# Optimization experiments

Hardware: AMD Instinct MI355X
Metric: run time of the kernel (lower is better)

## Reference

```python
import jax, jax.numpy as jnp
import numpy as np

EPS = 1e-5

def _conv1x1_bn(x, W, b, g, beta):
    # 1x1 conv == channel matmul; BN in training mode uses batch stats over (N,H,W)
    y = jnp.einsum('bchw,oc->bohw', x, W) + b[None, :, None, None]
    mu = jnp.mean(y, axis=(0, 2, 3))
    var = jnp.var(y, axis=(0, 2, 3))
    y = (y - mu[None, :, None, None]) * jax.lax.rsqrt(var + EPS)[None, :, None, None]
    return y * g[None, :, None, None] + beta[None, :, None, None]


def setup_inputs() -> dict:
    key = jax.random.key(0)
    ks = jax.random.split(key, 7)
    b, c, h, w = 8, 256, 64, 64
    sc = 1.0 / np.sqrt(c)
    inp = {
        'x': jax.random.normal(ks[0], (b, c, h, w), jnp.float32),
        'Wq': jax.random.normal(ks[1], (c, c), jnp.float32) * sc,
        'bq': jax.random.normal(ks[2], (c,), jnp.float32) * 0.02,
        'gq': jnp.ones((c,), jnp.float32),
        'betaq': jnp.zeros((c,), jnp.float32),
        'Wk': jax.random.normal(ks[3], (c, c), jnp.float32) * sc,
        'bk': jax.random.normal(ks[4], (c,), jnp.float32) * 0.02,
        'gk': jnp.ones((c,), jnp.float32),
        'betak': jnp.zeros((c,), jnp.float32),
        'Wv': jax.random.normal(ks[5], (c, c), jnp.float32) * sc,
        'bv': jax.random.normal(ks[6], (c,), jnp.float32) * 0.02,
        'gv': jnp.ones((c,), jnp.float32),
        'betav': jnp.zeros((c,), jnp.float32),
    }
    return inp


def reference(x, Wq, bq, gq, betaq, Wk, bk, gk, betak, Wv, bv, gv, betav):
    b, c, h, w = x.shape
    scale = float(h) ** (-0.5)
    Q = _conv1x1_bn(x, Wq, bq, gq, betaq).reshape(b, c, h * w)
    K = _conv1x1_bn(x, Wk, bk, gk, betak).reshape(b, c, h * w)
    V = _conv1x1_bn(x, Wv, bv, gv, betav).reshape(b, c, h * w)
    # un-normalized attention (no softmax)
    pixelMap = jnp.einsum('bcq,bck->bqk', Q, K) * scale  # [b, N, N]
    out = jnp.einsum('bqk,bck->bcq', pixelMap, V)        # [b, c, N]
    return out.reshape(b, c, h, w)
```

## Files before the change

### kernel.cpp

```cpp
#include <hip/hip_runtime.h>
#include <hip/hip_bf16.h>


#define BB 8
#define CC 256
#define NPIX 4096
#define PTOT 32768
#define EPSV 1e-5f
#define SCALEV 0.125f

#define OFF_PG    0L
#define OFF_SP    6291456L
#define OFF_S     6324224L
#define OFF_GHAT  6326272L
#define OFF_XBAR  6391808L
#define OFF_WP    6392064L
#define OFF_WKTF  6588672L
#define OFF_WVTF  6654208L
#define OFF_CVEC  6719744L
#define OFF_ACC   6720512L
#define OFF_GBF   6732800L
#define OFF_WQT   6994944L
#define OFF_WKT   7027712L
#define OFF_WVB   7060480L
#define OFF_ZT    7093248L
#define OFF_FT    7126016L
#define OFF_TBF   7388160L

#define ACC_U    0
#define ACC_W    2048
#define ACC_Y    4096
#define ACC_R    4352
#define ACC_H    4608
#define ACC_G    6656
#define ACC_VG   8704
#define ACC_SCAL 10752
#define ACC_TOT  12288

typedef __attribute__((ext_vector_type(8))) short short8;
typedef __attribute__((ext_vector_type(4))) float f32x4;

#define MFMA16(a, b, c) __builtin_amdgcn_mfma_f32_16x16x32_bf16((a), (b), (c), 0, 0, 0)

__device__ __forceinline__ ushort f2bf(float f) {
    union { float f; unsigned u; } v; v.f = f;
    const unsigned r = (v.u + 0x7FFFu + ((v.u >> 16) & 1u)) >> 16;
    return (ushort)r;
}

__device__ __forceinline__ float bf2f(ushort u) {
    union { unsigned u; float f; } v; v.u = ((unsigned)u) << 16;
    return v.f;
}

__device__ __forceinline__ ushort2 f2bf2(float a, float b) {
    __hip_bfloat162 h = __float22bfloat162_rn(float2{a, b});
    union { __hip_bfloat162 h; ushort2 u; } v; v.h = h;
    return v.u;
}

__device__ __forceinline__ float block_reduce(float v, float* red, int tid) {
    red[tid] = v; __syncthreads();
    for (int st = 128; st > 0; st >>= 1) {
        if (tid < st) red[tid] += red[tid + st];
        __syncthreads();
    }
    float r = red[0]; __syncthreads();
    return r;
}

__device__ __forceinline__ float2 wred2(float a, float b, float* red8, int tid) {
    #pragma unroll
    for (int s = 32; s > 0; s >>= 1) {
        a += __shfl_xor(a, s);
        b += __shfl_xor(b, s);
    }
    if ((tid & 63) == 0) { red8[(tid >> 6) * 2] = a; red8[(tid >> 6) * 2 + 1] = b; }
    __syncthreads();
    const float ra = red8[0] + red8[2] + red8[4] + red8[6];
    const float rb = red8[1] + red8[3] + red8[5] + red8[7];
    __syncthreads();
    return float2{ra, rb};
}

__global__ __launch_bounds__(256, 2) void gram_mfma(const float* __restrict__ x,
                                                    float* __restrict__ Pg,
                                                    float* __restrict__ Sp,
                                                    float* __restrict__ Ghat,
                                                    float* __restrict__ Acc) {
    __shared__ __align__(16) ushort Ab[128 * 72];
    __shared__ __align__(16) ushort Bb[128 * 72];
    __shared__ float rs[128];
    const int tid = threadIdx.x;
    const int ks = blockIdx.x, b = blockIdx.y, tt = blockIdx.z;
    const int lb = (tt * 8 + b) * 16 + ks;
    if (lb < 64) {
        #pragma unroll
        for (int i = 0; i < 4; ++i) Ghat[lb * 1024 + i * 256 + tid] = 0.f;
    } else if (lb < 76) {
        const int base = (lb - 64) * 1024;
        #pragma unroll
        for (int i = 0; i < 4; ++i) Acc[base + i * 256 + tid] = 0.f;
    }
    const int it = (tt == 1) ? 1 : 0;
    const int jt = (tt == 0) ? 0 : 1;
    const bool diag = (tt < 2);
    const int i0 = it * 128, j0 = jt * 128, k0 = ks * 256;
    const float* xb = x + (long)b * CC * NPIX;
    const int c = tid & 15, rp = tid >> 4;
    const int wave = tid >> 6, lane = tid & 63;
    const int wr = (wave >> 1) * 64, wc = (wave & 1) * 64;
    const int m = lane & 15, q8 = (lane >> 4) * 8;

    if (tid < 128) rs[tid] = 0.f;
    float rloc[8] = {};
    f32x4 acc[4][4];
    #pragma unroll
    for (int a = 0; a < 4; ++a)
        #pragma unroll
        for (int q = 0; q < 4; ++q) acc[a][q] = (f32x4){0.f, 0.f, 0.f, 0.f};

    const float* Abase = xb + (long)i0 * NPIX + k0 + c * 4;
    const float* Bbase = xb + (long)j0 * NPIX + k0 + c * 4;

    float4 va[8], vb[8];
    #pragma unroll
    for (int pp = 0; pp < 8; ++pp)
        va[pp] = *(const float4*)&Abase[(long)(pp * 16 + rp) * NPIX];
    if (!diag) {
        #pragma unroll
        for (int pp = 0; pp < 8; ++pp)
            vb[pp] = *(const float4*)&Bbase[(long)(pp * 16 + rp) * NPIX];
    }

    for (int kc = 0; kc < 256; kc += 64) {
        __syncthreads();
        #pragma unroll
        for (int pp = 0; pp < 8; ++pp) {
            const int row = pp * 16 + rp;
            const float4 v = va[pp];
            rloc[pp] += v.x + v.y + v.z + v.w;
            const ushort2 w01 = f2bf2(v.x, v.y);
            const ushort2 w23 = f2bf2(v.z, v.w);
            ushort4 w; w.x = w01.x; w.y = w01.y; w.z = w23.x; w.w = w23.y;
            *(ushort4*)&Ab[row * 72 + c * 4] = w;
        }
        if (!diag) {
            #pragma unroll
            for (int pp = 0; pp < 8; ++pp) {
                const int row = pp * 16 + rp;
                const float4 v = vb[pp];
                const ushort2 w01 = f2bf2(v.x, v.y);
                const ushort2 w23 = f2bf2(v.z, v.w);
                ushort4 w; w.x = w01.x; w.y = w01.y; w.z = w23.x; w.w = w23.y;
                *(ushort4*)&Bb[row * 72 + c * 4] = w;
            }
        }
        const int kn = kc + 64;
        if (kn < 256) {
            #pragma unroll
            for (int pp = 0; pp < 8; ++pp)
                va[pp] = *(const float4*)&Abase[(long)(pp * 16 + rp) * NPIX + kn];
            if (!diag) {
                #pragma unroll
                for (int pp = 0; pp < 8; ++pp)
                    vb[pp] = *(const float4*)&Bbase[(long)(pp * 16 + rp) * NPIX + kn];
            }
        }
        __syncthreads();
        const ushort* Bsrc = diag ? Ab : Bb;
        #pragma unroll
        for (int kk = 0; kk < 2; ++kk) {
            short8 af[4], bfv[4];
            #pragma unroll
            for (int a = 0; a < 4; ++a)
                af[a] = *(const short8*)&Ab[(wr + a * 16 + m) * 72 + kk * 32 + q8];
            #pragma unroll
            for (int q = 0; q < 4; ++q)
                bfv[q] = *(const short8*)&Bsrc[(wc + q * 16 + m) * 72 + kk * 32 + q8];
            #pragma unroll
            for (int a = 0; a < 4; ++a)
                #pragma unroll
                for (int q = 0; q < 4; ++q)
                    acc[a][q] = MFMA16(af[a], bfv[q], acc[a][q]);
        }
    }
    if (diag) {
        #pragma unroll
        for (int pp = 0; pp < 8; ++pp) atomicAdd(&rs[pp * 16 + rp], rloc[pp]);
        __syncthreads();
        if (tid < 128) Sp[(((long)ks * 8 + b) * 2 + it) * 128 + tid] = rs[tid];
    }
    float* Pt = Pg + (((long)ks * 8 + b) * 3 + tt) * 16384;
    const int rq = (lane >> 4) * 4;
    #pragma unroll
    for (int a = 0; a < 4; ++a) {
        #pragma unroll
        for (int q = 0; q < 4; ++q) {
            const int col = wc + q * 16 + m;
            #pragma unroll
            for (int reg = 0; reg < 4; ++reg)
                Pt[(long)(wr + a * 16 + rq + reg) * 128 + col] = acc[a][q][reg];
        }
    }
}

__global__ __launch_bounds__(256) void reduce_mirror(const float* __restrict__ Pg,
                                                     const float* __restrict__ Sp,
                                                     ushort* __restrict__ Gbf,
                                                     float* __restrict__ Ghat,
                                                     float* __restrict__ S,
                                                     float* __restrict__ xbar) {
    const int blk = blockIdx.x, tid = threadIdx.x;
    if (blk == 384) {
        const int it2 = tid >> 7, rr = tid & 127;
        float xacc = 0.f;
        for (int b = 0; b < BB; ++b) {
            float acc = 0.f;
            #pragma unroll
            for (int ks = 0; ks < 16; ++ks)
                acc += Sp[(((long)ks * 8 + b) * 2 + it2) * 128 + rr];
            S[b * 256 + tid] = acc;
            xacc += acc;
        }
        xbar[tid] = xacc * (1.0f / PTOT);
        return;
    }
    __shared__ float tile[32][33];
    const int tt = blk >> 7;
    const int sub = (blk >> 3) & 15;
    const int b = blk & 7;
    const int sr = (sub >> 2) * 32, sc = (sub & 3) * 32;
    const int it = (tt == 1) ? 1 : 0;
    const int jt = (tt == 0) ? 0 : 1;
    const bool offd = (tt == 2);
    const int gi0 = it * 128 + sr, gj0 = jt * 128 + sc;
    const int r = tid >> 3, c4 = (tid & 7) * 4;
    const float inv = 1.0f / PTOT;

    float s0 = 0.f, s1 = 0.f, s2 = 0.f, s3 = 0.f;
    #pragma unroll
    for (int ks = 0; ks < 16; ++ks) {
        const float4 v = *(const float4*)&Pg[(((long)ks * 8 + b) * 3 + tt) * 16384
                                             + (long)(sr + r) * 128 + sc + c4];
        s0 += v.x; s1 += v.y; s2 += v.z; s3 += v.w;
    }
    ushort4 w;
    w.x = f2bf(s0); w.y = f2bf(s1); w.z = f2bf(s2); w.w = f2bf(s3);
    *(ushort4*)&Gbf[(long)b * 65536 + (long)(gi0 + r) * 256 + gj0 + c4] = w;
    float* gd = &Ghat[(long)(gi0 + r) * 256 + gj0 + c4];
    atomicAdd(gd + 0, s0 * inv);
    atomicAdd(gd + 1, s1 * inv);
    atomicAdd(gd + 2, s2 * inv);
    atomicAdd(gd + 3, s3 * inv);
    if (offd) {
        tile[r][c4 + 0] = s0; tile[r][c4 + 1] = s1;
        tile[r][c4 + 2] = s2; tile[r][c4 + 3] = s3;
        __syncthreads();
        const float t0 = tile[c4 + 0][r], t1 = tile[c4 + 1][r];
        const float t2 = tile[c4 + 2][r], t3 = tile[c4 + 3][r];
        ushort4 tw;
        tw.x = f2bf(t0); tw.y = f2bf(t1); tw.z = f2bf(t2); tw.w = f2bf(t3);
        *(ushort4*)&Gbf[(long)b * 65536 + (long)(gj0 + r) * 256 + gi0 + c4] = tw;
        float* gm = &Ghat[(long)(gj0 + r) * 256 + gi0 + c4];
        atomicAdd(gm + 0, t0 * inv);
        atomicAdd(gm + 1, t1 * inv);
        atomicAdd(gm + 2, t2 * inv);
        atomicAdd(gm + 3, t3 * inv);
    }
}

__global__ __launch_bounds__(256) void stats_quad(const float* __restrict__ Wq, const float* __restrict__ Wk,
                           const float* __restrict__ Wv, const float* __restrict__ Ghat,
                           const float* __restrict__ xbar,
                           const float* bq, const float* gq, const float* betaq,
                           const float* bk, const float* gk, const float* betak,
                           const float* bv, const float* gv, const float* betav,
                           float* __restrict__ Wp, float* __restrict__ cvec,
                           ushort* __restrict__ WqT, ushort* __restrict__ WkT,
                           ushort* __restrict__ Wvb, float* __restrict__ WkTf,
                           float* __restrict__ WvTf) {
    const int og = blockIdx.x, t = blockIdx.y, tid = threadIdx.x;
    const int o0 = og * 4;
    const float* Wt  = t == 0 ? Wq : (t == 1 ? Wk : Wv);
    const float* bt  = t == 0 ? bq : (t == 1 ? bk : bv);
    const float* gt  = t == 0 ? gq : (t == 1 ? gk : gv);
    const float* bet = t == 0 ? betaq : (t == 1 ? betak : betav);
    __shared__ float wrows[4][256];
    __shared__ float red8[8];
    #pragma unroll
    for (int i = 0; i < 4; ++i) wrows[i][tid] = Wt[(o0 + i) * 256 + tid];
    const float xb = xbar[tid];
    __syncthreads();
    const float* grow = Ghat + (long)tid * 256;
    float tj[4] = {0.f, 0.f, 0.f, 0.f};
    #pragma unroll 8
    for (int k = 0; k < 256; k += 4) {
        const float4 g = *(const float4*)&grow[k];
        #pragma unroll
        for (int i = 0; i < 4; ++i)
            tj[i] += g.x * wrows[i][k]     + g.y * wrows[i][k + 1]
                   + g.z * wrows[i][k + 2] + g.w * wrows[i][k + 3];
    }
    #pragma unroll
    for (int i = 0; i < 4; ++i) {
        const int o = o0 + i;
        const float wv = wrows[i][tid];
        const float2 qw = wred2(wv * tj[i], wv * xb, red8, tid);
        const float bo = bt[o];
        const float mu = qw.y + bo;
        const float var = qw.x + 2.f * bo * mu - bo * bo - mu * mu;
        const float a = gt[o] * rsqrtf(var + EPSV);
        const float wpv = a * wv;
        Wp[(long)t * 65536 + o * 256 + tid] = wpv;
        const ushort wb = f2bf(wpv);
        if (t == 0) {
            WqT[(long)tid * 256 + o] = wb;
        } else if (t == 1) {
            WkT[(long)tid * 256 + o] = wb;
            WkTf[(long)tid * 256 + o] = wpv;
        } else {
            Wvb[(long)o * 256 + tid] = wb;
            WvTf[(long)tid * 256 + o] = wpv;
        }
        if (tid == 0) cvec[t * 256 + o] = a * (bo - mu) + bet[o];
    }
}

__device__ __forceinline__ void gemm_tile0(const ushort* __restrict__ Ab,
                                           const ushort* __restrict__ Bb,
                                           ushort* __restrict__ Db,
                                           int m0, int n0, int tid) {
    const int wave = tid >> 6, lane = tid & 63;
    const int wr = (wave >> 1) * 64, wc = (wave & 1) * 64;
    const int m = lane & 15, q8 = (lane >> 4) * 8;
    f32x4 acc[4][4];
    #pragma unroll
    for (int a = 0; a < 4; ++a)
        #pragma unroll
        for (int q = 0; q < 4; ++q) acc[a][q] = (f32x4){0.f, 0.f, 0.f, 0.f};
    #pragma unroll
    for (int kk = 0; kk < 8; ++kk) {
        short8 af[4], bfv[4];
        #pragma unroll
        for (int a = 0; a < 4; ++a)
            af[a] = *(const short8*)&Ab[(long)(m0 + wr + a * 16 + m) * 256 + kk * 32 + q8];
        #pragma unroll
        for (int q = 0; q < 4; ++q)
            bfv[q] = *(const short8*)&Bb[(long)(n0 + wc + q * 16 + m) * 256 + kk * 32 + q8];
        #pragma unroll
        for (int a = 0; a < 4; ++a)
            #pragma unroll
            for (int q = 0; q < 4; ++q)
                acc[a][q] = MFMA16(af[a], bfv[q], acc[a][q]);
    }
    const int rq = (lane >> 4) * 4;
    #pragma unroll
    for (int a = 0; a < 4; ++a) {
        #pragma unroll
        for (int q = 0; q < 4; ++q) {
            const int col = n0 + wc + q * 16 + m;
            #pragma unroll
            for (int reg = 0; reg < 4; ++reg)
                Db[(long)col * 256 + (m0 + wr + a * 16 + rq + reg)] = f2bf(acc[a][q][reg]);
        }
    }
}

__global__ __launch_bounds__(256) void zmida(const ushort* __restrict__ WkT,
                                             const ushort* __restrict__ WqT,
                                             ushort* __restrict__ ZT,
                                             const float* __restrict__ Wp,
                                             const float* __restrict__ WkTf,
                                             const float* __restrict__ WvTf,
                                             const float* __restrict__ S,
                                             const float* __restrict__ cvec,
                                             float* __restrict__ Acc) {
    const int blk = blockIdx.x, tid = threadIdx.x;
    __shared__ float sa[64], sb[64];
    if (blk < 4) {
        gemm_tile0(WkT, WqT, ZT, (blk >> 1) * 128, (blk & 1) * 128, tid);
        return;
    }
    if (blk < 36) {
        const int b = (blk - 4) >> 2, j0 = ((blk - 4) & 3) * 64;
        if (tid < 64) sa[tid] = S[b * 256 + j0 + tid];
        __syncthreads();
        float uu = 0.f, ww = 0.f;
        #pragma unroll 8
        for (int i = 0; i < 64; ++i) {
            const float sv = sa[i];
            uu += WvTf[(long)(j0 + i) * 256 + tid] * sv;
            ww += WkTf[(long)(j0 + i) * 256 + tid] * sv;
        }
        atomicAdd(&Acc[ACC_U + b * 256 + tid], uu);
        atomicAdd(&Acc[ACC_W + b * 256 + tid], ww);
    } else {
        const int o0 = (blk - 36) * 64;
        if (tid < 64) { sa[tid] = cvec[o0 + tid]; sb[tid] = cvec[256 + o0 + tid]; }
        __syncthreads();
        float yy = 0.f, rr = 0.f;
        #pragma unroll 8
        for (int i = 0; i < 64; ++i) {
            yy += Wp[65536L + (long)(o0 + i) * 256 + tid] * sa[i];
            rr += Wp[(long)(o0 + i) * 256 + tid] * sb[i];
        }
        atomicAdd(&Acc[ACC_Y + tid], yy);
        atomicAdd(&Acc[ACC_R + tid], rr);
    }
}

__global__ __launch_bounds__(256) void bcF2(const ushort* __restrict__ Gbf,
                                            const ushort* __restrict__ ZT,
                                            ushort* __restrict__ FT,
                                            const float* __restrict__ Wp,
                                            const float* __restrict__ cvec,
                                            float* __restrict__ Acc) {
    const int blk = blockIdx.x, tid = threadIdx.x;
    __shared__ float sa[64];
    __shared__ float red[256];
    if (blk < 32) {
        const int bz = blk >> 2, t = blk & 3;
        gemm_tile0(Gbf + (long)bz * 65536, ZT, FT + (long)bz * 65536,
                   (t >> 1) * 128, (t & 1) * 128, tid);
        return;
    }
    if (blk < 64) {
        const int b = (blk - 32) >> 2, o0 = ((blk - 32) & 3) * 64;
        if (tid < 64) sa[tid] = Acc[ACC_W + b * 256 + o0 + tid];
        __syncthreads();
        float hh = 0.f;
        #pragma unroll 8
        for (int i = 0; i < 64; ++i)
            hh += Wp[(long)(o0 + i) * 256 + tid] * sa[i];
        atomicAdd(&Acc[ACC_H + b * 256 + tid], hh);
    } else if (blk < 96) {
        const int b = (blk - 64) >> 2, o0 = ((blk - 64) & 3) * 64;
        if (tid < 64) sa[tid] = Acc[ACC_Y + o0 + tid];
        __syncthreads();
        float gg = 0.f;
        #pragma unroll 8
        for (int i = 0; i < 64; ++i)
            gg += bf2f(Gbf[(long)b * 65536 + (long)(o0 + i) * 256 + tid]) * sa[i];
        atomicAdd(&Acc[ACC_G + b * 256 + tid], gg);
    } else {
        const float cq = cvec[tid], ck = cvec[256 + tid];
        const float dkq = block_reduce(cq * ck, red, tid);
        if (tid == 0) Acc[ACC_SCAL] = dkq;
        for (int b = 0; b < BB; ++b) {
            const float dwq = block_reduce(Acc[ACC_W + b * 256 + tid] * cq, red, tid);
            if (tid == 0) Acc[ACC_SCAL + 1 + b] = dwq;
        }
    }
}

__global__ __launch_bounds__(256) void tvg(const ushort* __restrict__ Wvb,
                                           const ushort* __restrict__ FT,
                                           ushort* __restrict__ Tbf,
                                           const float* __restrict__ WvTf,
                                           const float* __restrict__ cvec,
                                           float* __restrict__ Acc) {
    const int blk = blockIdx.x, tid = threadIdx.x;
    __shared__ float sa[64];
    if (blk < 32) {
        const int bz = blk >> 2, t = blk & 3;
        const int m0 = (t >> 1) * 128, n0 = (t & 1) * 128;
        const ushort* Fb = FT + (long)bz * 65536;
        const int wave = tid >> 6, lane = tid & 63;
        const int wr = (wave >> 1) * 64, wc = (wave & 1) * 64;
        const int m = lane & 15, q8 = (lane >> 4) * 8;
        f32x4 acc[4][4];
        #pragma unroll
        for (int a = 0; a < 4; ++a)
            #pragma unroll
            for (int q = 0; q < 4; ++q) acc[a][q] = (f32x4){0.f, 0.f, 0.f, 0.f};
        #pragma unroll
        for (int kk = 0; kk < 8; ++kk) {
            short8 af[4], bfv[4];
            #pragma unroll
            for (int a = 0; a < 4; ++a)
                af[a] = *(const short8*)&Wvb[(long)(m0 + wr + a * 16 + m) * 256 + kk * 32 + q8];
            #pragma unroll
            for (int q = 0; q < 4; ++q)
                bfv[q] = *(const short8*)&Fb[(long)(n0 + wc + q * 16 + m) * 256 + kk * 32 + q8];
            #pragma unroll
            for (int a = 0; a < 4; ++a)
                #pragma unroll
                for (int q = 0; q < 4; ++q)
                    acc[a][q] = MFMA16(af[a], bfv[q], acc[a][q]);
        }
        const int rq = (lane >> 4) * 4;
        #pragma unroll
        for (int a = 0; a < 4; ++a) {
            #pragma unroll
            for (int q = 0; q < 4; ++q) {
                const int col = n0 + wc + q * 16 + m;
                const float rv = Acc[ACC_R + col];
                const float t2 = Acc[ACC_H + bz * 256 + col] + 4096.0f * rv;
                #pragma unroll
                for (int reg = 0; reg < 4; ++reg) {
                    const int row = m0 + wr + a * 16 + rq + reg;
                    const float val = SCALEV * (acc[a][q][reg]
                                                + Acc[ACC_U + bz * 256 + row] * rv
                                                + cvec[512 + row] * t2);
                    Tbf[(long)bz * 65536 + (long)row * 256 + col] = f2bf(val);
                }
            }
        }
    } else {
        const int b = (blk - 32) >> 2, j0 = ((blk - 32) & 3) * 64;
        if (tid < 64) sa[tid] = Acc[ACC_G + b * 256 + j0 + tid];
        __syncthreads();
        float vg = 0.f;
        #pragma unroll 8
        for (int i = 0; i < 64; ++i)
            vg += WvTf[(long)(j0 + i) * 256 + tid] * sa[i];
        atomicAdd(&Acc[ACC_VG + b * 256 + tid], vg);
    }
}

__global__ __launch_bounds__(256) void out_mfma(const ushort* __restrict__ Tbf,
                                                const float* __restrict__ x,
                                                const float* __restrict__ Acc,
                                                const float* __restrict__ cvec,
                                                float* __restrict__ out) {
    __shared__ __align__(16) ushort Bs[64 * 264];
    const int tid = threadIdx.x;
    const int p0 = blockIdx.x * 64;
    const int b = blockIdx.y;
    const float* xb = x + (long)b * CC * NPIX;
    const ushort* Tb = Tbf + (long)b * 65536;
    const float dkq = Acc[ACC_SCAL];
    const float dwqb = Acc[ACC_SCAL + 1 + b];

    const int c = tid & 15, kq = tid >> 4;
    #pragma unroll
    for (int kt = 0; kt < 4; ++kt) {
        const int k4 = kt * 64 + kq * 4;
        const int p = c * 4;
        const float4 v0 = *(const float4*)&xb[(long)(k4 + 0) * NPIX + p0 + p];
        const float4 v1 = *(const float4*)&xb[(long)(k4 + 1) * NPIX + p0 + p];
        const float4 v2 = *(const float4*)&xb[(long)(k4 + 2) * NPIX + p0 + p];
        const float4 v3 = *(const float4*)&xb[(long)(k4 + 3) * NPIX + p0 + p];
        ushort2 a01, a23;
        ushort4 w;
        a01 = f2bf2(v0.x, v1.x); a23 = f2bf2(v2.x, v3.x);
        w.x = a01.x; w.y = a01.y; w.z = a23.x; w.w = a23.y;
        *(ushort4*)&Bs[(p + 0) * 264 + k4] = w;
        a01 = f2bf2(v0.y, v1.y); a23 = f2bf2(v2.y, v3.y);
        w.x = a01.x; w.y = a01.y; w.z = a23.x; w.w = a23.y;
        *(ushort4*)&Bs[(p + 1) * 264 + k4] = w;
        a01 = f2bf2(v0.z, v1.z); a23 = f2bf2(v2.z, v3.z);
        w.x = a01.x; w.y = a01.y; w.z = a23.x; w.w = a23.y;
        *(ushort4*)&Bs[(p + 2) * 264 + k4] = w;
        a01 = f2bf2(v0.w, v1.w); a23 = f2bf2(v2.w, v3.w);
        w.x = a01.x; w.y = a01.y; w.z = a23.x; w.w = a23.y;
        *(ushort4*)&Bs[(p + 3) * 264 + k4] = w;
    }
    __syncthreads();

    const int wave = tid >> 6, lane = tid & 63;
    const int wr = wave * 64;
    const int m = lane & 15, q8 = (lane >> 4) * 8;
    f32x4 acc[4][4];
    #pragma unroll
    for (int a = 0; a < 4; ++a)
        #pragma unroll
        for (int q = 0; q < 4; ++q) acc[a][q] = (f32x4){0.f, 0.f, 0.f, 0.f};

    #pragma unroll
    for (int kk = 0; kk < 8; ++kk) {
        short8 af[4], bfv[4];
        #pragma unroll
        for (int a = 0; a < 4; ++a)
            af[a] = *(const short8*)&Tb[(long)(wr + a * 16 + m) * 256 + kk * 32 + q8];
        #pragma unroll
        for (int q = 0; q < 4; ++q)
            bfv[q] = *(const short8*)&Bs[(q * 16 + m) * 264 + kk * 32 + q8];
        #pragma unroll
        for (int a = 0; a < 4; ++a)
            #pragma unroll
            for (int q = 0; q < 4; ++q)
                acc[a][q] = MFMA16(af[a], bfv[q], acc[a][q]);
    }

    const int rq = (lane >> 4) * 4;
    #pragma unroll
    for (int a = 0; a < 4; ++a) {
        #pragma unroll
        for (int reg = 0; reg < 4; ++reg) {
            const int row = wr + a * 16 + rq + reg;
            const float off_ = SCALEV * (Acc[ACC_VG + b * 256 + row]
                                         + Acc[ACC_U + b * 256 + row] * dkq
                                         + cvec[512 + row] * (dwqb + 4096.0f * dkq));
            float* orow = &out[((long)b * CC + row) * NPIX + p0];
            #pragma unroll
            for (int q = 0; q < 4; ++q)
                orow[q * 16 + m] = acc[a][q][reg] + off_;
        }
    }
}

extern "C" void kernel_launch(void* const* d_in, const int* in_sizes, int n_in,
                              void* d_out, int out_size, void* d_ws, size_t ws_size,
                              hipStream_t stream) {
    const float* x     = (const float*)d_in[0];
    const float* Wq    = (const float*)d_in[1];
    const float* bq    = (const float*)d_in[2];
    const float* gq    = (const float*)d_in[3];
    const float* betaq = (const float*)d_in[4];
    const float* Wk    = (const float*)d_in[5];
    const float* bk    = (const float*)d_in[6];
    const float* gk    = (const float*)d_in[7];
    const float* betak = (const float*)d_in[8];
    const float* Wv    = (const float*)d_in[9];
    const float* bv    = (const float*)d_in[10];
    const float* gv    = (const float*)d_in[11];
    const float* betav = (const float*)d_in[12];
    float* ws = (float*)d_ws;

    float*  Pg   = ws + OFF_PG;
    float*  Sp   = ws + OFF_SP;
    float*  S    = ws + OFF_S;
    float*  Ghat = ws + OFF_GHAT;
    float*  Xbar = ws + OFF_XBAR;
    float*  Wp   = ws + OFF_WP;
    float*  WkTf = ws + OFF_WKTF;
    float*  WvTf = ws + OFF_WVTF;
    float*  cvec = ws + OFF_CVEC;
    float*  Acc  = ws + OFF_ACC;
    ushort* Gbf  = (ushort*)(ws + OFF_GBF);
    ushort* WqT  = (ushort*)(ws + OFF_WQT);
    ushort* WkT  = (ushort*)(ws + OFF_WKT);
    ushort* Wvb  = (ushort*)(ws + OFF_WVB);
    ushort* ZT   = (ushort*)(ws + OFF_ZT);
    ushort* FT   = (ushort*)(ws + OFF_FT);
    ushort* Tbf  = (ushort*)(ws + OFF_TBF);

    gram_mfma<<<dim3(16, 8, 3), 256, 0, stream>>>(x, Pg, Sp, Ghat, Acc);
    reduce_mirror<<<385, 256, 0, stream>>>(Pg, Sp, Gbf, Ghat, S, Xbar);
    stats_quad<<<dim3(64, 3), 256, 0, stream>>>(Wq, Wk, Wv, Ghat, Xbar,
                                                bq, gq, betaq, bk, gk, betak,
                                                bv, gv, betav, Wp, cvec,
                                                WqT, WkT, Wvb, WkTf, WvTf);
    zmida<<<40, 256, 0, stream>>>(WkT, WqT, ZT, Wp, WkTf, WvTf, S, cvec, Acc);
    bcF2<<<97, 256, 0, stream>>>(Gbf, ZT, FT, Wp, cvec, Acc);
    tvg<<<64, 256, 0, stream>>>(Wvb, FT, Tbf, WvTf, cvec, Acc);
    out_mfma<<<dim3(64, 8), 256, 0, stream>>>(Tbf, x, Acc, cvec, (float*)d_out);
}
```

Baseline: 190.1 us.

## Load Gram MFMA fragments directly from global memory, bypassing LDS staging

The Gram kernel no longer stages x tiles through shared memory. Each lane loads its MFMA fragment rows straight from global memory as float4 pairs, packs them to bf16 in registers, and reduces row sums with wave shuffles. Partial Gram tiles are now stored transposed as vector f32x4 writes, and the reduce kernel reads and transposes them to match. This removes LDS traffic and barriers, but each wave re-reads overlapping rows from global or L2 and loses the explicit register prefetch pipeline.

```diff
diff --git a/kernel.cpp b/kernel.cpp
--- a/kernel.cpp
+++ b/kernel.cpp
@@ -59,6 +59,15 @@
     return v.u;
 }
 
+__device__ __forceinline__ short8 pack8(const float4 u0, const float4 u1) {
+    union { short8 s; ushort2 u2[4]; } t;
+    t.u2[0] = f2bf2(u0.x, u0.y);
+    t.u2[1] = f2bf2(u0.z, u0.w);
+    t.u2[2] = f2bf2(u1.x, u1.y);
+    t.u2[3] = f2bf2(u1.z, u1.w);
+    return t.s;
+}
+
 __device__ __forceinline__ float block_reduce(float v, float* red, int tid) {
     red[tid] = v; __syncthreads();
     for (int st = 128; st > 0; st >>= 1) {
@@ -88,8 +97,6 @@
                                                     float* __restrict__ Sp,
                                                     float* __restrict__ Ghat,
                                                     float* __restrict__ Acc) {
-    __shared__ __align__(16) ushort Ab[128 * 72];
-    __shared__ __align__(16) ushort Bb[128 * 72];
     __shared__ float rs[128];
     const int tid = threadIdx.x;
     const int ks = blockIdx.x, b = blockIdx.y, tt = blockIdx.z;
@@ -107,90 +114,60 @@
     const bool diag = (tt < 2);
     const int i0 = it * 128, j0 = jt * 128, k0 = ks * 256;
     const float* xb = x + (long)b * CC * NPIX;
-    const int c = tid & 15, rp = tid >> 4;
     const int wave = tid >> 6, lane = tid & 63;
     const int wr = (wave >> 1) * 64, wc = (wave & 1) * 64;
     const int m = lane & 15, q8 = (lane >> 4) * 8;
 
-    if (tid < 128) rs[tid] = 0.f;
-    float rloc[8] = {};
+    const float* Arow = xb + (long)i0 * NPIX + k0;
+    const float* Brow = xb + (long)(diag ? i0 : j0) * NPIX + k0;
+
     f32x4 acc[4][4];
     #pragma unroll
     for (int a = 0; a < 4; ++a)
         #pragma unroll
         for (int q = 0; q < 4; ++q) acc[a][q] = (f32x4){0.f, 0.f, 0.f, 0.f};
-
-    const float* Abase = xb + (long)i0 * NPIX + k0 + c * 4;
-    const float* Bbase = xb + (long)j0 * NPIX + k0 + c * 4;
-
-    float4 va[8], vb[8];
-    #pragma unroll
-    for (int pp = 0; pp < 8; ++pp)
-        va[pp] = *(const float4*)&Abase[(long)(pp * 16 + rp) * NPIX];
-    if (!diag) {
-        #pragma unroll
-        for (int pp = 0; pp < 8; ++pp)
-            vb[pp] = *(const float4*)&Bbase[(long)(pp * 16 + rp) * NPIX];
-    }
-
-    for (int kc = 0; kc < 256; kc += 64) {
-        __syncthreads();
-        #pragma unroll
-        for (int pp = 0; pp < 8; ++pp) {
-            const int row = pp * 16 + rp;
-            const float4 v = va[pp];
-            rloc[pp] += v.x + v.y + v.z + v.w;
-            const ushort2 w01 = f2bf2(v.x, v.y);
-            const ushort2 w23 = f2bf2(v.z, v.w);
-            ushort4 w; w.x = w01.x; w.y = w01.y; w.z = w23.x; w.w = w23.y;
-            *(ushort4*)&Ab[row * 72 + c * 4] = w;
-        }
-        if (!diag) {
-            #pragma unroll
-            for (int pp = 0; pp < 8; ++pp) {
-                const int row = pp * 16 + rp;
-                const float4 v = vb[pp];
-                const ushort2 w01 = f2bf2(v.x, v.y);
-                const ushort2 w23 = f2bf2(v.z, v.w);
-                ushort4 w; w.x = w01.x; w.y = w01.y; w.z = w23.x; w.w = w23.y;
-                *(ushort4*)&Bb[row * 72 + c * 4] = w;
-            }
-        }
-        const int kn = kc + 64;
-        if (kn < 256) {
-            #pragma unroll
-            for (int pp = 0; pp < 8; ++pp)
-                va[pp] = *(const float4*)&Abase[(long)(pp * 16 + rp) * NPIX + kn];
-            if (!diag) {
-                #pragma unroll
-                for (int pp = 0; pp < 8; ++pp)
-                    vb[pp] = *(const float4*)&Bbase[(long)(pp * 16 + rp) * NPIX + kn];
-            }
-        }
-        __syncthreads();
-        const ushort* Bsrc = diag ? Ab : Bb;
-        #pragma unroll
-        for (int kk = 0; kk < 2; ++kk) {
-            short8 af[4], bfv[4];
-            #pragma unroll
-            for (int a = 0; a < 4; ++a)
-                af[a] = *(const short8*)&Ab[(wr + a * 16 + m) * 72 + kk * 32 + q8];
+    float rsum[4] = {0.f, 0.f, 0.f, 0.f};
+
+    #pragma unroll
+    for (int kk = 0; kk < 8; ++kk) {
+        const int kb = kk * 32 + q8;
+        short8 af[4], bfv[4];
+        #pragma unroll
+        for (int a = 0; a < 4; ++a) {
+            const long ro = (long)(wr + a * 16 + m) * NPIX + kb;
+            const float4 u0 = *(const float4*)&Arow[ro];
+            const float4 u1 = *(const float4*)&Arow[ro + 4];
+            rsum[a] += u0.x + u0.y + u0.z + u0.w + u1.x + u1.y + u1.z + u1.w;
+            af[a] = pack8(u0, u1);
+        }
+        #pragma unroll
+        for (int q = 0; q < 4; ++q) {
+            const long ro = (long)(wc + q * 16 + m) * NPIX + kb;
+            const float4 u0 = *(const float4*)&Brow[ro];
+            const float4 u1 = *(const float4*)&Brow[ro + 4];
+            bfv[q] = pack8(u0, u1);
+        }
+        #pragma unroll
+        for (int a = 0; a < 4; ++a)
             #pragma unroll
             for (int q = 0; q < 4; ++q)
-                bfv[q] = *(const short8*)&Bsrc[(wc + q * 16 + m) * 72 + kk * 32 + q8];
-            #pragma unroll
-            for (int a = 0; a < 4; ++a)
-                #pragma unroll
-                for (int q = 0; q < 4; ++q)
-                    acc[a][q] = MFMA16(af[a], bfv[q], acc[a][q]);
-        }
-    }
+                acc[a][q] = MFMA16(af[a], bfv[q], acc[a][q]);
+    }
+
     if (diag) {
         #pragma unroll
-        for (int pp = 0; pp < 8; ++pp) atomicAdd(&rs[pp * 16 + rp], rloc[pp]);
+        for (int a = 0; a < 4; ++a) {
+            rsum[a] += __shfl_xor(rsum[a], 16);
+            rsum[a] += __shfl_xor(rsum[a], 32);
+        }
+        if (((wave & 1) == 0) && ((lane >> 4) == 0)) {
+            #pragma unroll
+            for (int a = 0; a < 4; ++a) rs[wr + a * 16 + m] = rsum[a];
+        }
         __syncthreads();
         if (tid < 128) Sp[(((long)ks * 8 + b) * 2 + it) * 128 + tid] = rs[tid];
     }
+
     float* Pt = Pg + (((long)ks * 8 + b) * 3 + tt) * 16384;
     const int rq = (lane >> 4) * 4;
     #pragma unroll
@@ -198,9 +175,7 @@
         #pragma unroll
         for (int q = 0; q < 4; ++q) {
             const int col = wc + q * 16 + m;
-            #pragma unroll
-            for (int reg = 0; reg < 4; ++reg)
-                Pt[(long)(wr + a * 16 + rq + reg) * 128 + col] = acc[a][q][reg];
+            *(f32x4*)&Pt[(long)col * 128 + wr + a * 16 + rq] = acc[a][q];
         }
     }
 }
@@ -235,38 +210,38 @@
     const int jt = (tt == 0) ? 0 : 1;
     const bool offd = (tt == 2);
     const int gi0 = it * 128 + sr, gj0 = jt * 128 + sc;
-    const int r = tid >> 3, c4 = (tid & 7) * 4;
+    const int rr = tid >> 3, c4 = (tid & 7) * 4;
     const float inv = 1.0f / PTOT;
 
     float s0 = 0.f, s1 = 0.f, s2 = 0.f, s3 = 0.f;
     #pragma unroll
     for (int ks = 0; ks < 16; ++ks) {
         const float4 v = *(const float4*)&Pg[(((long)ks * 8 + b) * 3 + tt) * 16384
-                                             + (long)(sr + r) * 128 + sc + c4];
+                                             + (long)(sc + rr) * 128 + sr + c4];
         s0 += v.x; s1 += v.y; s2 += v.z; s3 += v.w;
     }
+    tile[c4 + 0][rr] = s0; tile[c4 + 1][rr] = s1;
+    tile[c4 + 2][rr] = s2; tile[c4 + 3][rr] = s3;
+    __syncthreads();
+    const float t0 = tile[rr][c4 + 0], t1 = tile[rr][c4 + 1];
+    const float t2 = tile[rr][c4 + 2], t3 = tile[rr][c4 + 3];
     ushort4 w;
-    w.x = f2bf(s0); w.y = f2bf(s1); w.z = f2bf(s2); w.w = f2bf(s3);
-    *(ushort4*)&Gbf[(long)b * 65536 + (long)(gi0 + r) * 256 + gj0 + c4] = w;
-    float* gd = &Ghat[(long)(gi0 + r) * 256 + gj0 + c4];
-    atomicAdd(gd + 0, s0 * inv);
-    atomicAdd(gd + 1, s1 * inv);
-    atomicAdd(gd + 2, s2 * inv);
-    atomicAdd(gd + 3, s3 * inv);
+    w.x = f2bf(t0); w.y = f2bf(t1); w.z = f2bf(t2); w.w = f2bf(t3);
+    *(ushort4*)&Gbf[(long)b * 65536 + (long)(gi0 + rr) * 256 + gj0 + c4] = w;
+    float* gd = &Ghat[(long)(gi0 + rr) * 256 + gj0 + c4];
+    atomicAdd(gd + 0, t0 * inv);
+    atomicAdd(gd + 1, t1 * inv);
+    atomicAdd(gd + 2, t2 * inv);
+    atomicAdd(gd + 3, t3 * inv);
     if (offd) {
-        tile[r][c4 + 0] = s0; tile[r][c4 + 1] = s1;
-        tile[r][c4 + 2] = s2; tile[r][c4 + 3] = s3;
-        __syncthreads();
-        const float t0 = tile[c4 + 0][r], t1 = tile[c4 + 1][r];
-        const float t2 = tile[c4 + 2][r], t3 = tile[c4 + 3][r];
         ushort4 tw;
-        tw.x = f2bf(t0); tw.y = f2bf(t1); tw.z = f2bf(t2); tw.w = f2bf(t3);
-        *(ushort4*)&Gbf[(long)b * 65536 + (long)(gj0 + r) * 256 + gi0 + c4] = tw;
-        float* gm = &Ghat[(long)(gj0 + r) * 256 + gi0 + c4];
-        atomicAdd(gm + 0, t0 * inv);
-        atomicAdd(gm + 1, t1 * inv);
-        atomicAdd(gm + 2, t2 * inv);
-        atomicAdd(gm + 3, t3 * inv);
+        tw.x = f2bf(s0); tw.y = f2bf(s1); tw.z = f2bf(s2); tw.w = f2bf(s3);
+        *(ushort4*)&Gbf[(long)b * 65536 + (long)(gj0 + rr) * 256 + gi0 + c4] = tw;
+        float* gm = &Ghat[(long)(gj0 + rr) * 256 + gi0 + c4];
+        atomicAdd(gm + 0, s0 * inv);
+        atomicAdd(gm + 1, s1 * inv);
+        atomicAdd(gm + 2, s2 * inv);
+        atomicAdd(gm + 3, s3 * inv);
     }
 }
 
```

Measured after the change: 244.2 us. 1.28x slower.
